# Optimization experiments

Hardware: AMD Instinct MI355X
Metric: run time of the kernel (lower is better)

## Reference

```python
import jax, jax.numpy as jnp
import numpy as np
from jax import lax

S = 24  # number of depth slices / groups

def setup_inputs() -> dict:
    key = jax.random.key(0)
    k1, k2, k3 = jax.random.split(key, 3)
    x = jax.random.normal(k1, (8, 1, S, 256, 256), dtype=jnp.float32)
    # PyTorch ConvTranspose2d weight layout: [in_ch=1, out_ch=1, kH=4, kW=4], stacked over 24 slices
    w = jax.random.normal(k2, (S, 1, 1, 4, 4), dtype=jnp.float32) * 0.25  # ~ pytorch init scale
    b = jax.random.normal(k3, (S,), dtype=jnp.float32) * 0.25
    return {"x": x, "w": w, "b": b}

def _fwd(x, w, b):
    # x: [B, 1, S, H, W] -> treat the S slices as 24 groups of a single grouped
    # transposed conv (fuses the original loop of 24 tiny ConvTranspose2d ops).
    B, C, s, H, W = x.shape
    xs = x.reshape(B, s, H, W)  # [B, S, H, W], channel dim = S
    # transposed conv == dilated conv with spatially-flipped kernel,
    # padding = k - 1 - p = 4 - 1 - 1 = 2 on each side, lhs_dilation = stride = 2
    wf = w[:, 0, 0, ::-1, ::-1][:, None]  # [S, 1, 4, 4] OIHW, groups=S
    y = lax.conv_general_dilated(
        xs, wf,
        window_strides=(1, 1),
        padding=((2, 2), (2, 2)),
        lhs_dilation=(2, 2),
        dimension_numbers=("NCHW", "OIHW", "NCHW"),
        feature_group_count=s,
    )  # [B, S, 2H, 2W]
    y = y + b[None, :, None, None]
    return y[:, None]  # [B, 1, S, 2H, 2W]

def reference(x, w, b):
    return _fwd(x, w, b)
```

## Files before the change

kernel.cpp:

```cpp
#include <hip/hip_runtime.h>


#define NS 24
#define IH 256
#define IW 256
#define OHH 512
#define OWW 512

typedef float f32x4 __attribute__((ext_vector_type(4)));

__global__ __launch_bounds__(256) void convt2x_coal_kernel(
    const float* __restrict__ x, const float* __restrict__ w,
    const float* __restrict__ bias, float* __restrict__ out)
{
    const int b  = blockIdx.z;
    const int s  = blockIdx.y;
    const int xr  = ((blockIdx.x & 7) << 3) | (blockIdx.x >> 3);
    const int lin = xr * 256 + threadIdx.x;
    const int t   = lin & 63;
    const int r   = lin >> 6;

    const float* ximg = x + (size_t)(b * NS + s) * IH * IW;

    const float* wv = w + s * 16;
    float W[16];
    #pragma unroll
    for (int k = 0; k < 16; ++k) W[k] = wv[k];
    const float bb = bias[s];

    float X[3][2][4];
    #pragma unroll
    for (int i = 0; i < 3; ++i) {
        const int rr = r - 1 + i;
        float2 mA = make_float2(0.f, 0.f);
        float2 mB = make_float2(0.f, 0.f);
        if (rr >= 0 && rr < IH) {
            const float* row = ximg + (size_t)rr * IW;
            mA = *(const float2*)(row + 2 * t);
            mB = *(const float2*)(row + 128 + 2 * t);
        }
        const float sAy = __shfl(mA.y, (t - 1) & 63);
        const float sAx = __shfl(mA.x, (t + 1) & 63);
        const float sBy = __shfl(mB.y, (t - 1) & 63);
        const float sBx = __shfl(mB.x, (t + 1) & 63);
        const float c127 = __shfl(mA.y, 63);
        const float c128 = __shfl(mB.x, 0);

        X[i][0][0] = (t == 0)  ? 0.f  : sAy;
        X[i][0][1] = mA.x;
        X[i][0][2] = mA.y;
        X[i][0][3] = (t == 63) ? c128 : sAx;
        X[i][1][0] = (t == 0)  ? c127 : sBy;
        X[i][1][1] = mB.x;
        X[i][1][2] = mB.y;
        X[i][1][3] = (t == 63) ? 0.f  : sBx;
    }

    float o0[2][4], o1[2][4];
    #pragma unroll
    for (int z = 0; z < 2; ++z) {
        o0[z][0] = X[0][z][0]*W[15] + X[0][z][1]*W[13]
                 + X[1][z][0]*W[7]  + X[1][z][1]*W[5]  + bb;
        o0[z][1] = X[0][z][1]*W[14] + X[0][z][2]*W[12]
                 + X[1][z][1]*W[6]  + X[1][z][2]*W[4]  + bb;
        o0[z][2] = X[0][z][1]*W[15] + X[0][z][2]*W[13]
                 + X[1][z][1]*W[7]  + X[1][z][2]*W[5]  + bb;
        o0[z][3] = X[0][z][2]*W[14] + X[0][z][3]*W[12]
                 + X[1][z][2]*W[6]  + X[1][z][3]*W[4]  + bb;
        o1[z][0] = X[1][z][0]*W[11] + X[1][z][1]*W[9]
                 + X[2][z][0]*W[3]  + X[2][z][1]*W[1]  + bb;
        o1[z][1] = X[1][z][1]*W[10] + X[1][z][2]*W[8]
                 + X[2][z][1]*W[2]  + X[2][z][2]*W[0]  + bb;
        o1[z][2] = X[1][z][1]*W[11] + X[1][z][2]*W[9]
                 + X[2][z][1]*W[3]  + X[2][z][2]*W[1]  + bb;
        o1[z][3] = X[1][z][2]*W[10] + X[1][z][3]*W[8]
                 + X[2][z][2]*W[2]  + X[2][z][3]*W[0]  + bb;
    }

    float* obase = out + ((size_t)(b * NS + s) * OHH + 2 * r) * OWW;
    #pragma unroll
    for (int z = 0; z < 2; ++z) {
        f32x4 v0 = { o0[z][0], o0[z][1], o0[z][2], o0[z][3] };
        f32x4 v1 = { o1[z][0], o1[z][1], o1[z][2], o1[z][3] };
        __builtin_nontemporal_store(v0, (f32x4*)(obase + z * 256 + 4 * t));
        __builtin_nontemporal_store(v1, (f32x4*)(obase + OWW + z * 256 + 4 * t));
    }
}

extern "C" void kernel_launch(void* const* d_in, const int* in_sizes, int n_in,
                              void* d_out, int out_size, void* d_ws, size_t ws_size,
                              hipStream_t stream) {
    const float* x    = (const float*)d_in[0];
    const float* w    = (const float*)d_in[1];
    const float* bias = (const float*)d_in[2];
    float* out        = (float*)d_out;

    dim3 grid(64, NS, 8);
    convt2x_coal_kernel<<<grid, 256, 0, stream>>>(x, w, bias, out);
}
```

Before: 238.4 us.

## Process four rows per warp with rolling register window for input reuse

Each warp now computes four consecutive input rows, keeping a rotating three-row register window so each input row is loaded and shuffled once instead of three times. The grid shrinks by four in the x dimension accordingly. This cuts redundant global loads and shuffle work, but lowers block count and lengthens each thread's serial chain of loads and stores.

New measurement: 238.5 us (median of 2 runs). No clear change (+0.0%).

```diff
diff --git a/kernel.cpp b/kernel.cpp
--- a/kernel.cpp
+++ b/kernel.cpp
@@ -6,19 +6,47 @@
 #define IW 256
 #define OHH 512
 #define OWW 512
+#define RP 4
 
 typedef float f32x4 __attribute__((ext_vector_type(4)));
 
-__global__ __launch_bounds__(256) void convt2x_coal_kernel(
+__device__ __forceinline__ void load_row(const float* __restrict__ ximg,
+                                         int rr, int t, float v[2][4])
+{
+    float2 mA = make_float2(0.f, 0.f);
+    float2 mB = make_float2(0.f, 0.f);
+    if (rr >= 0 && rr < IH) {
+        const float* row = ximg + (size_t)rr * IW;
+        mA = *(const float2*)(row + 2 * t);
+        mB = *(const float2*)(row + 128 + 2 * t);
+    }
+    const float sAy = __shfl(mA.y, (t - 1) & 63);
+    const float sAx = __shfl(mA.x, (t + 1) & 63);
+    const float sBy = __shfl(mB.y, (t - 1) & 63);
+    const float sBx = __shfl(mB.x, (t + 1) & 63);
+    const float c127 = __shfl(mA.y, 63);
+    const float c128 = __shfl(mB.x, 0);
+
+    v[0][0] = (t == 0)  ? 0.f  : sAy;
+    v[0][1] = mA.x;
+    v[0][2] = mA.y;
+    v[0][3] = (t == 63) ? c128 : sAx;
+    v[1][0] = (t == 0)  ? c127 : sBy;
+    v[1][1] = mB.x;
+    v[1][2] = mB.y;
+    v[1][3] = (t == 63) ? 0.f  : sBx;
+}
+
+__global__ __launch_bounds__(256) void convt2x_roll_kernel(
     const float* __restrict__ x, const float* __restrict__ w,
     const float* __restrict__ bias, float* __restrict__ out)
 {
-    const int b  = blockIdx.z;
-    const int s  = blockIdx.y;
-    const int xr  = ((blockIdx.x & 7) << 3) | (blockIdx.x >> 3);
-    const int lin = xr * 256 + threadIdx.x;
-    const int t   = lin & 63;
-    const int r   = lin >> 6;
+    const int b   = blockIdx.z;
+    const int s   = blockIdx.y;
+    const int xr  = ((blockIdx.x & 7) << 1) | (blockIdx.x >> 3);
+    const int t   = threadIdx.x & 63;
+    const int wid = threadIdx.x >> 6;
+    const int r0  = xr * 16 + wid * 4;
 
     const float* ximg = x + (size_t)(b * NS + s) * IH * IW;
 
@@ -29,61 +57,47 @@
     const float bb = bias[s];
 
     float X[3][2][4];
+    load_row(ximg, r0 - 1, t, X[0]);
+    load_row(ximg, r0,     t, X[1]);
+
     #pragma unroll
-    for (int i = 0; i < 3; ++i) {
-        const int rr = r - 1 + i;
-        float2 mA = make_float2(0.f, 0.f);
-        float2 mB = make_float2(0.f, 0.f);
-        if (rr >= 0 && rr < IH) {
-            const float* row = ximg + (size_t)rr * IW;
-            mA = *(const float2*)(row + 2 * t);
-            mB = *(const float2*)(row + 128 + 2 * t);
+    for (int p = 0; p < RP; ++p) {
+        const int r = r0 + p;
+        load_row(ximg, r + 1, t, X[(p + 2) % 3]);
+
+        float (&T)[2][4] = X[(p + 0) % 3];
+        float (&M)[2][4] = X[(p + 1) % 3];
+        float (&B)[2][4] = X[(p + 2) % 3];
+
+        float o0[2][4], o1[2][4];
+        #pragma unroll
+        for (int z = 0; z < 2; ++z) {
+            o0[z][0] = T[z][0]*W[15] + T[z][1]*W[13]
+                     + M[z][0]*W[7]  + M[z][1]*W[5]  + bb;
+            o0[z][1] = T[z][1]*W[14] + T[z][2]*W[12]
+                     + M[z][1]*W[6]  + M[z][2]*W[4]  + bb;
+            o0[z][2] = T[z][1]*W[15] + T[z][2]*W[13]
+                     + M[z][1]*W[7]  + M[z][2]*W[5]  + bb;
+            o0[z][3] = T[z][2]*W[14] + T[z][3]*W[12]
+                     + M[z][2]*W[6]  + M[z][3]*W[4]  + bb;
+            o1[z][0] = M[z][0]*W[11] + M[z][1]*W[9]
+                     + B[z][0]*W[3]  + B[z][1]*W[1]  + bb;
+            o1[z][1] = M[z][1]*W[10] + M[z][2]*W[8]
+                     + B[z][1]*W[2]  + B[z][2]*W[0]  + bb;
+            o1[z][2] = M[z][1]*W[11] + M[z][2]*W[9]
+                     + B[z][1]*W[3]  + B[z][2]*W[1]  + bb;
+            o1[z][3] = M[z][2]*W[10] + M[z][3]*W[8]
+                     + B[z][2]*W[2]  + B[z][3]*W[0]  + bb;
         }
-        const float sAy = __shfl(mA.y, (t - 1) & 63);
-        const float sAx = __shfl(mA.x, (t + 1) & 63);
-        const float sBy = __shfl(mB.y, (t - 1) & 63);
-        const float sBx = __shfl(mB.x, (t + 1) & 63);
-        const float c127 = __shfl(mA.y, 63);
-        const float c128 = __shfl(mB.x, 0);
 
-        X[i][0][0] = (t == 0)  ? 0.f  : sAy;
-        X[i][0][1] = mA.x;
-        X[i][0][2] = mA.y;
-        X[i][0][3] = (t == 63) ? c128 : sAx;
-        X[i][1][0] = (t == 0)  ? c127 : sBy;
-        X[i][1][1] = mB.x;
-        X[i][1][2] = mB.y;
-        X[i][1][3] = (t == 63) ? 0.f  : sBx;
-    }
-
-    float o0[2][4], o1[2][4];
-    #pragma unroll
-    for (int z = 0; z < 2; ++z) {
-        o0[z][0] = X[0][z][0]*W[15] + X[0][z][1]*W[13]
-                 + X[1][z][0]*W[7]  + X[1][z][1]*W[5]  + bb;
-        o0[z][1] = X[0][z][1]*W[14] + X[0][z][2]*W[12]
-                 + X[1][z][1]*W[6]  + X[1][z][2]*W[4]  + bb;
-        o0[z][2] = X[0][z][1]*W[15] + X[0][z][2]*W[13]
-                 + X[1][z][1]*W[7]  + X[1][z][2]*W[5]  + bb;
-        o0[z][3] = X[0][z][2]*W[14] + X[0][z][3]*W[12]
-                 + X[1][z][2]*W[6]  + X[1][z][3]*W[4]  + bb;
-        o1[z][0] = X[1][z][0]*W[11] + X[1][z][1]*W[9]
-                 + X[2][z][0]*W[3]  + X[2][z][1]*W[1]  + bb;
-        o1[z][1] = X[1][z][1]*W[10] + X[1][z][2]*W[8]
-                 + X[2][z][1]*W[2]  + X[2][z][2]*W[0]  + bb;
-        o1[z][2] = X[1][z][1]*W[11] + X[1][z][2]*W[9]
-                 + X[2][z][1]*W[3]  + X[2][z][2]*W[1]  + bb;
-        o1[z][3] = X[1][z][2]*W[10] + X[1][z][3]*W[8]
-                 + X[2][z][2]*W[2]  + X[2][z][3]*W[0]  + bb;
-    }
-
-    float* obase = out + ((size_t)(b * NS + s) * OHH + 2 * r) * OWW;
-    #pragma unroll
-    for (int z = 0; z < 2; ++z) {
-        f32x4 v0 = { o0[z][0], o0[z][1], o0[z][2], o0[z][3] };
-        f32x4 v1 = { o1[z][0], o1[z][1], o1[z][2], o1[z][3] };
-        __builtin_nontemporal_store(v0, (f32x4*)(obase + z * 256 + 4 * t));
-        __builtin_nontemporal_store(v1, (f32x4*)(obase + OWW + z * 256 + 4 * t));
+        float* obase = out + ((size_t)(b * NS + s) * OHH + 2 * r) * OWW;
+        #pragma unroll
+        for (int z = 0; z < 2; ++z) {
+            f32x4 v0 = { o0[z][0], o0[z][1], o0[z][2], o0[z][3] };
+            f32x4 v1 = { o1[z][0], o1[z][1], o1[z][2], o1[z][3] };
+            __builtin_nontemporal_store(v0, (f32x4*)(obase + z * 256 + 4 * t));
+            __builtin_nontemporal_store(v1, (f32x4*)(obase + OWW + z * 256 + 4 * t));
+        }
     }
 }
 
@@ -95,6 +109,6 @@
     const float* bias = (const float*)d_in[2];
     float* out        = (float*)d_out;
 
-    dim3 grid(64, NS, 8);
-    convt2x_coal_kernel<<<grid, 256, 0, stream>>>(x, w, bias, out);
+    dim3 grid(16, NS, 8);
+    convt2x_roll_kernel<<<grid, 256, 0, stream>>>(x, w, bias, out);
 }
```
